# Kernel optimization log

Measured on AMD Instinct MI355X. Metric: run time of the kernel, lower is better.

The kernel has to match this reference:

```python
import jax, jax.numpy as jnp
import numpy as np

B, C, L = 16, 256, 2048

def setup_inputs() -> dict:
    key = jax.random.key(0)
    k1, k2, k3, k4 = jax.random.split(key, 4)
    return {
        "proj_query": jax.random.normal(k1, (B, C, L), dtype=jnp.float32),
        "proj_key": jax.random.normal(k2, (B, C, L), dtype=jnp.float32),
        "proj_val": jax.random.normal(k3, (B, C, L), dtype=jnp.float32),
        "padding_mask": jax.random.uniform(k4, (B, 1, L), dtype=jnp.float32),
    }

def reference(proj_query, proj_key, proj_val, padding_mask):
    c = proj_query.shape[1]
    # energy[b,l,m] = sum_c Q[b,c,l] * K[b,c,m]  -> (B, L, L)
    energy = jnp.einsum("bcl,bcm->blm", proj_query, proj_key) / jnp.sqrt(jnp.float32(c))
    # log-additive padding mask (the tril mask in the source is dead code, never applied)
    logits = energy + jnp.log(padding_mask + 1e-9)
    attention = jax.nn.softmax(logits, axis=-1)
    # post-softmax multiplicative mask
    attention = attention * padding_mask
    # out[b,c,l] = sum_m V[b,c,m] * attention[b,l,m]  -> (B, C, L)
    out = jnp.einsum("bcm,blm->bcl", proj_val, attention)
    return out
```

## Files before the change

### kernel.cpp

```cpp
#include <hip/hip_runtime.h>
#include <hip/hip_bf16.h>

#define B_ 16
#define C_ 256
#define L_ 2048
#define KVB 32
#define NT (L_ / KVB)

typedef __attribute__((ext_vector_type(8))) short bf16x8;
typedef __attribute__((ext_vector_type(4))) unsigned u32x4;
typedef __attribute__((ext_vector_type(16))) float f32x16;

#define CEXP 0.09016844005556021f

__device__ __forceinline__ short f2bf_rne(float f) {
    union { float f; unsigned u; } x; x.f = f;
    unsigned r = x.u + 0x7fffu + ((x.u >> 16) & 1u);
    return (short)(r >> 16);
}

__device__ __forceinline__ unsigned pack2(float lo, float hi) {
    return (unsigned)(unsigned short)f2bf_rne(lo)
         | ((unsigned)(unsigned short)f2bf_rne(hi) << 16);
}

__device__ __forceinline__ void gld_lds16(const void* g, void* l) {
    __builtin_amdgcn_global_load_lds(
        (const __attribute__((address_space(1))) void*)g,
        (__attribute__((address_space(3))) void*)l, 16, 0, 0);
}

__global__ __launch_bounds__(256) void prepass_kernel(
        const float* __restrict__ Kin, const float* __restrict__ Vin,
        const float* __restrict__ mask,
        short* __restrict__ Kt, short* __restrict__ Vb) {
    const int bid = blockIdx.x;
    const int t = threadIdx.x;
    if (bid < 512) {
        __shared__ unsigned short tile[64 * 256];
        const int b  = bid >> 5;
        const int l0 = (bid & 31) * 64;
        #pragma unroll
        for (int iter = 0; iter < 16; ++iter) {
            int idx = iter * 256 + t;
            int ci = idx >> 4;
            int lc = (idx & 15) * 4;
            float4 v = *(const float4*)(Kin + ((size_t)(b * C_ + ci)) * L_ + l0 + lc);
            float vv[4] = {v.x, v.y, v.z, v.w};
            #pragma unroll
            for (int j = 0; j < 4; ++j) {
                int l = lc + j;
                tile[l * 256 + (((ci >> 3) ^ (l & 31)) << 3) + (ci & 7)] =
                    (unsigned short)f2bf_rne(vv[j]);
            }
        }
        __syncthreads();
        #pragma unroll
        for (int iter = 0; iter < 8; ++iter) {
            int li = iter * 8 + (t >> 5);
            int ck = t & 31;
            uint4 val = *(const uint4*)(tile + li * 256 + ((ck ^ (li & 31)) << 3));
            *(uint4*)(Kt + ((size_t)(b * L_ + l0 + li)) * C_ + ck * 8) = val;
        }
    } else {
        size_t e = ((size_t)(bid - 512) * 256 + t) * 8;
        int b = (int)(e >> 19);
        int m = (int)(e & (L_ - 1));
        const float4 v0 = *(const float4*)(Vin + e);
        const float4 v1 = *(const float4*)(Vin + e + 4);
        const float* mp = mask + ((size_t)b << 11) + m;
        const float4 m0 = *(const float4*)mp;
        const float4 m1 = *(const float4*)(mp + 4);
        uint4 o;
        o.x = (unsigned)(unsigned short)f2bf_rne(v0.x * m0.x)
            | ((unsigned)(unsigned short)f2bf_rne(v0.y * m0.y) << 16);
        o.y = (unsigned)(unsigned short)f2bf_rne(v0.z * m0.z)
            | ((unsigned)(unsigned short)f2bf_rne(v0.w * m0.w) << 16);
        o.z = (unsigned)(unsigned short)f2bf_rne(v1.x * m1.x)
            | ((unsigned)(unsigned short)f2bf_rne(v1.y * m1.y) << 16);
        o.w = (unsigned)(unsigned short)f2bf_rne(v1.z * m1.z)
            | ((unsigned)(unsigned short)f2bf_rne(v1.w * m1.w) << 16);
        *(uint4*)(Vb + e) = o;
    }
}

__device__ __forceinline__ void stage_K(const short* __restrict__ Ksrc,
                                        short* Ks, int m0, int t) {
    #pragma unroll
    for (int rr = 0; rr < 4; ++rr) {
        int G = rr * 256 + t;
        int m = G >> 5, p = G & 31;
        gld_lds16(Ksrc + ((size_t)(m0 + m) << 8) + ((p ^ m) << 3), Ks + G * 8);
    }
}

__device__ __forceinline__ void stage_V(const short* __restrict__ Vsrc,
                                        short* Vs, int m0, int t) {
    #pragma unroll
    for (int rr = 0; rr < 4; ++rr) {
        int G = rr * 256 + t;
        int c = G >> 2, p = G & 3;
        gld_lds16(Vsrc + (size_t)c * L_ + m0 + ((p ^ (c & 3)) << 3), Vs + G * 8);
    }
}

#define TILE_BODY(KS, VS, M0)                                                               \
  {                                                                                         \
    const short* Krow = (KS) + ln * 256;                                                    \
    bf16x8 kf[16];                                                                          \
    _Pragma("unroll")                                                                       \
    for (int ki = 0; ki < 16; ++ki)                                                         \
      kf[ki] = *(const bf16x8*)(Krow + (((2 * ki + h) ^ ln) << 3));                         \
    float4 mk[4];                                                                           \
    _Pragma("unroll")                                                                       \
    for (int s = 0; s < 4; ++s) mk[s] = *(const float4*)(mrow + (M0) + 8 * s + 4 * h);      \
    f32x16 s0 = z16, s1 = z16;                                                              \
    _Pragma("unroll")                                                                       \
    for (int ki = 0; ki < 8; ++ki)                                                          \
      s0 = __builtin_amdgcn_mfma_f32_32x32x16_bf16(kf[ki], qf[ki], s0, 0, 0, 0);            \
    _Pragma("unroll")                                                                       \
    for (int ki = 8; ki < 16; ++ki)                                                         \
      s1 = __builtin_amdgcn_mfma_f32_32x32x16_bf16(kf[ki], qf[ki], s1, 0, 0, 0);            \
    unsigned wds[8];                                                                        \
    _Pragma("unroll")                                                                       \
    for (int u = 0; u < 8; ++u) {                                                           \
      const int ra = 2 * u, rb = 2 * u + 1;                                                 \
      float fa = (mk[ra >> 2][ra & 3] + 1e-9f) * exp2f(s0[ra] + s1[ra]);                    \
      float fb = (mk[rb >> 2][rb & 3] + 1e-9f) * exp2f(s0[rb] + s1[rb]);                    \
      dn += fa + fb;                                                                        \
      wds[u] = pack2(fa, fb);                                                               \
    }                                                                                       \
    unsigned e0 = __shfl_xor(h ? wds[0] : wds[2], 32, 64);                                  \
    unsigned e1 = __shfl_xor(h ? wds[1] : wds[3], 32, 64);                                  \
    unsigned e2 = __shfl_xor(h ? wds[4] : wds[6], 32, 64);                                  \
    unsigned e3 = __shfl_xor(h ? wds[5] : wds[7], 32, 64);                                  \
    u32x4 b1u = { h ? e0 : wds[0], h ? e1 : wds[1], h ? wds[2] : e0, h ? wds[3] : e1 };     \
    u32x4 b2u = { h ? e2 : wds[4], h ? e3 : wds[5], h ? wds[6] : e2, h ? wds[7] : e3 };     \
    bf16x8 b1 = __builtin_bit_cast(bf16x8, b1u);                                            \
    bf16x8 b2 = __builtin_bit_cast(bf16x8, b2u);                                            \
    _Pragma("unroll")                                                                       \
    for (int ct = 0; ct < 8; ++ct) {                                                        \
      const short* Vrow = (VS) + (32 * ct + ln) * 32;                                       \
      bf16x8 av1 = *(const bf16x8*)(Vrow + ((h ^ (ln & 3)) << 3));                          \
      bf16x8 av2 = *(const bf16x8*)(Vrow + (((2 + h) ^ (ln & 3)) << 3));                    \
      Oacc[ct] = __builtin_amdgcn_mfma_f32_32x32x16_bf16(av1, b1, Oacc[ct], 0, 0, 0);       \
      Oacc[ct] = __builtin_amdgcn_mfma_f32_32x32x16_bf16(av2, b2, Oacc[ct], 0, 0, 0);       \
    }                                                                                       \
  }

__global__ __launch_bounds__(256, 1) void attn_main(
        const float* __restrict__ Qin,
        const short* __restrict__ Kt,
        const short* __restrict__ Vb,
        const float* __restrict__ mask,
        float* __restrict__ out) {
    __shared__ __align__(16) char smem[65536];
    short* KsB0 = (short*)smem;
    short* KsB1 = (short*)(smem + 16384);
    short* VsB0 = (short*)(smem + 32768);
    short* VsB1 = (short*)(smem + 49152);

    const int t = threadIdx.x;
    const int w = t >> 6, lane = t & 63;
    const int ln = lane & 31, h = lane >> 5;

    const int b  = blockIdx.x & 15;
    const int l0 = (blockIdx.x >> 4) * 128;
    const int lw = l0 + 32 * w;

    const short* Ksrc = Kt + (size_t)b * (L_ * C_);
    const short* Vsrc = Vb + (size_t)b * (C_ * L_);
    const float* mrow = mask + (size_t)b * L_;

    stage_K(Ksrc, KsB0, 0, t);
    stage_V(Vsrc, VsB0, 0, t);

    bf16x8 qf[16];
    {
        const float* Qb = Qin + (size_t)b * (C_ * L_) + (lw + ln);
        #pragma unroll
        for (int ki = 0; ki < 16; ++ki) {
            bf16x8 v;
            #pragma unroll
            for (int j = 0; j < 8; ++j) {
                float f = Qb[(size_t)(16 * ki + 8 * h + j) * L_];
                v[j] = f2bf_rne(f * CEXP);
            }
            qf[ki] = v;
        }
    }

    const f32x16 z16 = {0.f,0.f,0.f,0.f,0.f,0.f,0.f,0.f,0.f,0.f,0.f,0.f,0.f,0.f,0.f,0.f};
    f32x16 Oacc[8];
    #pragma unroll
    for (int ct = 0; ct < 8; ++ct) Oacc[ct] = z16;
    float dn = 0.f;

    __syncthreads();

    #pragma unroll 1
    for (int it2 = 0; it2 < NT / 2; ++it2) {
        const int m0a = it2 * (2 * KVB);
        const int m0b = m0a + KVB;

        stage_K(Ksrc, KsB1, m0b, t);
        stage_V(Vsrc, VsB1, m0b, t);
        TILE_BODY(KsB0, VsB0, m0a)
        __syncthreads();

        if (m0b + KVB < L_) {
            stage_K(Ksrc, KsB0, m0b + KVB, t);
            stage_V(Vsrc, VsB0, m0b + KVB, t);
        }
        TILE_BODY(KsB1, VsB1, m0b)
        __syncthreads();
    }

    dn += __shfl_xor(dn, 32, 64);
    const float rden = 1.0f / dn;

    float* ob = out + (size_t)b * (C_ * L_) + lw + ln;
    #pragma unroll
    for (int ct = 0; ct < 8; ++ct)
        #pragma unroll
        for (int r = 0; r < 16; ++r) {
            int c = 32 * ct + (r & 3) + 8 * (r >> 2) + 4 * h;
            ob[(size_t)c * L_] = Oacc[ct][r] * rden;
        }
}

extern "C" void kernel_launch(void* const* d_in, const int* in_sizes, int n_in,
                              void* d_out, int out_size, void* d_ws, size_t ws_size,
                              hipStream_t stream) {
    const float* Q    = (const float*)d_in[0];
    const float* K    = (const float*)d_in[1];
    const float* V    = (const float*)d_in[2];
    const float* mask = (const float*)d_in[3];
    float* out = (float*)d_out;

    short* Kt = (short*)d_ws;
    short* Vb = Kt + (size_t)B_ * L_ * C_;

    prepass_kernel<<<4608, 256, 0, stream>>>(K, V, mask, Kt, Vb);
    attn_main<<<256, 256, 0, stream>>>(Q, Kt, Vb, mask, out);
}
```

Before: 244.3 us.

## Split KV range across wave pairs with LDS reduction of partial outputs

Doubles the block to 512 threads so each 32-row query slice is handled by two waves that process alternating KV tiles, staging two tiles per buffer and later summing the partial accumulators and denominators through shared memory. The goal is more waves per CU to hide latency, since the grid of 256 blocks only gave one wave per SIMD. It also changes the V LDS swizzle to reduce bank conflicts. In exchange it needs about 128KB of LDS per block and a shared-memory reduction epilogue, and launch_bounds(512,2) will not fit two blocks per CU.

```diff
diff --git a/kernel.cpp b/kernel.cpp
--- a/kernel.cpp
+++ b/kernel.cpp
@@ -87,8 +87,8 @@
 __device__ __forceinline__ void stage_K(const short* __restrict__ Ksrc,
                                         short* Ks, int m0, int t) {
     #pragma unroll
-    for (int rr = 0; rr < 4; ++rr) {
-        int G = rr * 256 + t;
+    for (int rr = 0; rr < 2; ++rr) {
+        int G = rr * 512 + t;
         int m = G >> 5, p = G & 31;
         gld_lds16(Ksrc + ((size_t)(m0 + m) << 8) + ((p ^ m) << 3), Ks + G * 8);
     }
@@ -97,10 +97,10 @@
 __device__ __forceinline__ void stage_V(const short* __restrict__ Vsrc,
                                         short* Vs, int m0, int t) {
     #pragma unroll
-    for (int rr = 0; rr < 4; ++rr) {
-        int G = rr * 256 + t;
+    for (int rr = 0; rr < 2; ++rr) {
+        int G = rr * 512 + t;
         int c = G >> 2, p = G & 3;
-        gld_lds16(Vsrc + (size_t)c * L_ + m0 + ((p ^ (c & 3)) << 3), Vs + G * 8);
+        gld_lds16(Vsrc + (size_t)c * L_ + m0 + ((p ^ ((c >> 1) & 3)) << 3), Vs + G * 8);
     }
 }
 
@@ -138,42 +138,52 @@
     u32x4 b2u = { h ? e2 : wds[4], h ? e3 : wds[5], h ? wds[6] : e2, h ? wds[7] : e3 };     \
     bf16x8 b1 = __builtin_bit_cast(bf16x8, b1u);                                            \
     bf16x8 b2 = __builtin_bit_cast(bf16x8, b2u);                                            \
+    const int vsw = (ln >> 1) & 3;                                                          \
     _Pragma("unroll")                                                                       \
     for (int ct = 0; ct < 8; ++ct) {                                                        \
       const short* Vrow = (VS) + (32 * ct + ln) * 32;                                       \
-      bf16x8 av1 = *(const bf16x8*)(Vrow + ((h ^ (ln & 3)) << 3));                          \
-      bf16x8 av2 = *(const bf16x8*)(Vrow + (((2 + h) ^ (ln & 3)) << 3));                    \
+      bf16x8 av1 = *(const bf16x8*)(Vrow + ((h ^ vsw) << 3));                               \
+      bf16x8 av2 = *(const bf16x8*)(Vrow + (((2 + h) ^ vsw) << 3));                         \
       Oacc[ct] = __builtin_amdgcn_mfma_f32_32x32x16_bf16(av1, b1, Oacc[ct], 0, 0, 0);       \
       Oacc[ct] = __builtin_amdgcn_mfma_f32_32x32x16_bf16(av2, b2, Oacc[ct], 0, 0, 0);       \
     }                                                                                       \
   }
 
-__global__ __launch_bounds__(256, 1) void attn_main(
+__global__ __launch_bounds__(512, 2) void attn_main(
         const float* __restrict__ Qin,
         const short* __restrict__ Kt,
         const short* __restrict__ Vb,
         const float* __restrict__ mask,
         float* __restrict__ out) {
-    __shared__ __align__(16) char smem[65536];
-    short* KsB0 = (short*)smem;
-    short* KsB1 = (short*)(smem + 16384);
-    short* VsB0 = (short*)(smem + 32768);
-    short* VsB1 = (short*)(smem + 49152);
+    __shared__ __align__(16) char smem[131584];
+    float* Dsh = (float*)(smem + 131072);
 
     const int t = threadIdx.x;
     const int w = t >> 6, lane = t & 63;
     const int ln = lane & 31, h = lane >> 5;
+    const int pr = w >> 1, e = w & 1;
 
     const int b  = blockIdx.x & 15;
     const int l0 = (blockIdx.x >> 4) * 128;
-    const int lw = l0 + 32 * w;
+    const int lw = l0 + 32 * pr;
 
     const short* Ksrc = Kt + (size_t)b * (L_ * C_);
     const short* Vsrc = Vb + (size_t)b * (C_ * L_);
     const float* mrow = mask + (size_t)b * L_;
 
-    stage_K(Ksrc, KsB0, 0, t);
-    stage_V(Vsrc, VsB0, 0, t);
+    short* KsP0 = (short*)smem + e * 8192;
+    short* KsP1 = (short*)(smem + 32768) + e * 8192;
+    short* VsP0 = (short*)(smem + 65536) + e * 8192;
+    short* VsP1 = (short*)(smem + 98304) + e * 8192;
+    short* KsB[2][2] = { {(short*)smem, (short*)(smem + 16384)},
+                         {(short*)(smem + 32768), (short*)(smem + 49152)} };
+    short* VsB[2][2] = { {(short*)(smem + 65536), (short*)(smem + 81920)},
+                         {(short*)(smem + 98304), (short*)(smem + 114688)} };
+
+    stage_K(Ksrc, KsB[0][0], 0, t);
+    stage_K(Ksrc, KsB[0][1], KVB, t);
+    stage_V(Vsrc, VsB[0][0], 0, t);
+    stage_V(Vsrc, VsB[0][1], KVB, t);
 
     bf16x8 qf[16];
     {
@@ -199,34 +209,59 @@
     __syncthreads();
 
     #pragma unroll 1
-    for (int it2 = 0; it2 < NT / 2; ++it2) {
-        const int m0a = it2 * (2 * KVB);
-        const int m0b = m0a + KVB;
-
-        stage_K(Ksrc, KsB1, m0b, t);
-        stage_V(Vsrc, VsB1, m0b, t);
-        TILE_BODY(KsB0, VsB0, m0a)
+    for (int it4 = 0; it4 < NT / 4; ++it4) {
+        const int m0 = it4 * (4 * KVB);
+
+        stage_K(Ksrc, KsB[1][0], m0 + 2 * KVB, t);
+        stage_K(Ksrc, KsB[1][1], m0 + 3 * KVB, t);
+        stage_V(Vsrc, VsB[1][0], m0 + 2 * KVB, t);
+        stage_V(Vsrc, VsB[1][1], m0 + 3 * KVB, t);
+        TILE_BODY(KsP0, VsP0, m0 + KVB * e)
         __syncthreads();
 
-        if (m0b + KVB < L_) {
-            stage_K(Ksrc, KsB0, m0b + KVB, t);
-            stage_V(Vsrc, VsB0, m0b + KVB, t);
-        }
-        TILE_BODY(KsB1, VsB1, m0b)
+        if (it4 + 1 < NT / 4) {
+            stage_K(Ksrc, KsB[0][0], m0 + 4 * KVB, t);
+            stage_K(Ksrc, KsB[0][1], m0 + 5 * KVB, t);
+            stage_V(Vsrc, VsB[0][0], m0 + 4 * KVB, t);
+            stage_V(Vsrc, VsB[0][1], m0 + 5 * KVB, t);
+        }
+        TILE_BODY(KsP1, VsP1, m0 + 2 * KVB + KVB * e)
         __syncthreads();
     }
 
     dn += __shfl_xor(dn, 32, 64);
-    const float rden = 1.0f / dn;
-
-    float* ob = out + (size_t)b * (C_ * L_) + lw + ln;
-    #pragma unroll
-    for (int ct = 0; ct < 8; ++ct)
-        #pragma unroll
-        for (int r = 0; r < 16; ++r) {
-            int c = 32 * ct + (r & 3) + 8 * (r >> 2) + 4 * h;
-            ob[(size_t)c * L_] = Oacc[ct][r] * rden;
-        }
+
+    if (e) {
+        char* Ob = smem + pr * 32768;
+        #pragma unroll
+        for (int ct = 0; ct < 8; ++ct)
+            #pragma unroll
+            for (int rq = 0; rq < 4; ++rq) {
+                float4 v4 = { Oacc[ct][4*rq+0], Oacc[ct][4*rq+1],
+                              Oacc[ct][4*rq+2], Oacc[ct][4*rq+3] };
+                *(float4*)(Ob + lane * 512 + (((ct * 4 + rq) ^ (lane & 31)) << 4)) = v4;
+            }
+        if (h == 0) Dsh[pr * 32 + ln] = dn;
+    }
+    __syncthreads();
+    if (!e) {
+        dn += Dsh[pr * 32 + ln];
+        const float rden = 1.0f / dn;
+        const char* Ob = smem + pr * 32768;
+        float* ob = out + (size_t)b * (C_ * L_) + lw + ln;
+        #pragma unroll
+        for (int ct = 0; ct < 8; ++ct)
+            #pragma unroll
+            for (int rq = 0; rq < 4; ++rq) {
+                float4 p4 = *(const float4*)(Ob + lane * 512 + (((ct * 4 + rq) ^ (lane & 31)) << 4));
+                #pragma unroll
+                for (int j = 0; j < 4; ++j) {
+                    int r = 4 * rq + j;
+                    int c = 32 * ct + (r & 3) + 8 * (r >> 2) + 4 * h;
+                    ob[(size_t)c * L_] = (Oacc[ct][r] + ((const float*)&p4)[j]) * rden;
+                }
+            }
+    }
 }
 
 extern "C" void kernel_launch(void* const* d_in, const int* in_sizes, int n_in,
@@ -242,5 +277,5 @@
     short* Vb = Kt + (size_t)B_ * L_ * C_;
 
     prepass_kernel<<<4608, 256, 0, stream>>>(K, V, mask, Kt, Vb);
-    attn_main<<<256, 256, 0, stream>>>(Q, Kt, Vb, mask, out);
-}
+    attn_main<<<256, 512, 0, stream>>>(Q, Kt, Vb, mask, out);
+}
```

Measured after the change: 293.3 us. 1.2x slower.
